# Performance work log

Hardware: AMD Instinct MI355X
Metric: run time of the kernel (lower is better)

The kernel has to match this reference:

```python
import jax, jax.numpy as jnp
import numpy as np

N_NODES = 100000
N_EDGES = 1600000
N_GRAPHS = 1000
NODES_PER_GRAPH = 100  # batch vector is arange(N)//100: exactly 100 nodes per graph
HID = 32
MAX_Z = 1000
K = 30
D_LAT = HID * 3 + 1  # 97, total_latent_dim


def setup_inputs() -> dict:
    key = jax.random.key(0)
    ks = jax.random.split(key, 24)
    s = 1.0 / np.sqrt(HID)
    inp = {
        "z": jax.random.randint(ks[0], (N_NODES,), 0, MAX_Z, dtype=jnp.int32),
        "edge_index": jax.random.randint(ks[1], (2, N_EDGES), 0, N_NODES, dtype=jnp.int32),
        "batch": (jnp.arange(N_NODES, dtype=jnp.int32) // NODES_PER_GRAPH),
        "edge_weight": jax.random.uniform(ks[2], (N_EDGES,), jnp.float32, 0.1, 1.0),
        "z_emb": jax.random.normal(ks[3], (MAX_Z, HID), jnp.float32) * 0.1,
        # GCNConv stack: [32->32, 32->32, 32->32, 32->1]
        "Wg1": jax.random.normal(ks[4], (HID, HID)) * s,
        "bg1": jnp.zeros((HID,), jnp.float32),
        "Wg2": jax.random.normal(ks[5], (HID, HID)) * s,
        "bg2": jnp.zeros((HID,), jnp.float32),
        "Wg3": jax.random.normal(ks[6], (HID, HID)) * s,
        "bg3": jnp.zeros((HID,), jnp.float32),
        "Wg4": jax.random.normal(ks[7], (HID, 1)) * s,
        "bg4": jnp.zeros((1,), jnp.float32),
        # Conv1d(1, 16, kernel=97, stride=97)
        "Wc1": jax.random.normal(ks[8], (16, D_LAT)) * (1.0 / np.sqrt(D_LAT)),
        "bc1": jnp.zeros((16,), jnp.float32),
        # Conv1d(16, 32, kernel=5, stride=1)
        "Wc2": jax.random.normal(ks[9], (32, 16, 5)) * (1.0 / np.sqrt(16 * 5)),
        "bc2": jnp.zeros((32,), jnp.float32),
        # Linear(352, 128), Linear(128, 1)
        "Wl1": jax.random.normal(ks[10], (352, 128)) * (1.0 / np.sqrt(352)),
        "bl1": jnp.zeros((128,), jnp.float32),
        "Wl2": jax.random.normal(ks[11], (128, 1)) * (1.0 / np.sqrt(128)),
        "bl2": jnp.zeros((1,), jnp.float32),
    }
    return inp


def gcn_conv(x, src, dst, ew, W, b, n):
    # PyG GCNConv: xW, add self-loops (weight 1), sym-normalize, aggregate at dst, + bias
    xw = x @ W
    deg = jax.ops.segment_sum(ew, dst, num_segments=n) + 1.0  # +1 for self loop
    dinv = jnp.where(deg > 0, jax.lax.rsqrt(deg), 0.0)
    norm = dinv[src] * ew * dinv[dst]                          # [E]
    out = jax.ops.segment_sum(norm[:, None] * xw[src], dst, num_segments=n)
    out = out + xw * (dinv * dinv)[:, None]                    # self-loop term
    return out + b


def _forward(z, edge_index, batch, edge_weight, z_emb, Wg1, bg1, Wg2, bg2, Wg3, bg3,
             Wg4, bg4, Wc1, bc1, Wc2, bc2, Wl1, bl1, Wl2, bl2):
    src, dst = edge_index[0], edge_index[1]
    n = z.shape[0]
    x = z_emb[z]                                              # [N, 32]
    xs = []
    h = x
    for W, b in ((Wg1, bg1), (Wg2, bg2), (Wg3, bg3), (Wg4, bg4)):
        h = jnp.tanh(gcn_conv(h, src, dst, edge_weight, W, b, n))
        xs.append(h)
    x = jnp.concatenate(xs, axis=-1)                          # [N, 97]
    # global_sort_pool: batch is uniform (100 nodes/graph) so dense batching is a reshape
    dense = x.reshape(N_GRAPHS, NODES_PER_GRAPH, D_LAT)       # [B, 100, 97]
    idx = jnp.argsort(-dense[:, :, -1], axis=1)[:, :K]        # sort desc by last channel
    top = jnp.take_along_axis(dense, idx[:, :, None], axis=1)  # [B, 30, 97]
    # Conv1d(1,16,97,stride=97) on flattened [B,1,30*97] == per-slot dense layer
    y = jax.nn.relu(jnp.einsum('bkd,cd->bck', top, Wc1) + bc1[None, :, None])  # [B,16,30]
    y = y.reshape(N_GRAPHS, 16, K // 2, 2).max(axis=-1)        # MaxPool1d(2,2) -> [B,16,15]
    y = jax.lax.conv_general_dilated(y, Wc2, (1,), 'VALID',
                                     dimension_numbers=('NCH', 'OIH', 'NCH'))
    y = jax.nn.relu(y + bc2[None, :, None])                    # [B,32,11]
    y = y.reshape(N_GRAPHS, -1)                                # [B,352]
    y = jax.nn.relu(y @ Wl1 + bl1)                             # dropout: eval mode, identity
    return y @ Wl2 + bl2                                       # [B,1]


def reference(z, edge_index, batch, edge_weight, z_emb, Wg1, bg1, Wg2, bg2, Wg3, bg3,
              Wg4, bg4, Wc1, bc1, Wc2, bc2, Wl1, bl1, Wl2, bl2):
    return _forward(z, edge_index, batch, edge_weight, z_emb, Wg1, bg1, Wg2, bg2, Wg3,
                    bg3, Wg4, bg4, Wc1, bc1, Wc2, bc2, Wl1, bl1, Wl2, bl2)
```

## Files before the change

### kernel.cpp

```cpp
#include <hip/hip_runtime.h>

#define HID 32
#define DLAT 97
#define NPG 100
#define TOPK 30
#define BKT_NODES 128
#define BKT_SHIFT 7
#define NBUCK 1024
#define CAPF 2432
#define CHUNK 8192

typedef float f32x4 __attribute__((ext_vector_type(4)));

__device__ __forceinline__ f32x4 gload4(const float* p) {
    f32x4 r;
    asm volatile("global_load_dwordx4 %0, %1, off" : "=v"(r) : "v"(p));
    return r;
}

__global__ __launch_bounds__(512) void binB1_kernel(
    const int* __restrict__ src, const int* __restrict__ dst,
    const float* __restrict__ ew, int* __restrict__ gcursor,
    int2* __restrict__ bedge, int E) {
    __shared__ int hist[NBUCK];
    __shared__ int lcur[NBUCK];
    __shared__ int dcache[CHUNK];
    for (int i = threadIdx.x; i < NBUCK; i += 512) hist[i] = 0;
    __syncthreads();
    int base = blockIdx.x * CHUNK;
    int M = min(E - base, CHUNK);
    for (int i = threadIdx.x; i < M; i += 512) {
        int d = dst[base + i];
        dcache[i] = d;
        atomicAdd(&hist[d >> BKT_SHIFT], 1);
    }
    __syncthreads();
    for (int b = threadIdx.x; b < NBUCK; b += 512) {
        int v = hist[b];
        lcur[b] = b * CAPF + (v ? atomicAdd(&gcursor[b], v) : 0);
    }
    __syncthreads();
    for (int i = threadIdx.x; i < M; i += 512) {
        int d = dcache[i];
        int slot = atomicAdd(&lcur[d >> BKT_SHIFT], 1);
        bedge[slot] = make_int2(src[base + i] | ((d & (BKT_NODES - 1)) << 20),
                                __float_as_int(ew[base + i]));
    }
}

__global__ __launch_bounds__(256) void scan1024_kernel(
    const int* __restrict__ g, int* __restrict__ bstart) {
    __shared__ int sh[256];
    int t = threadIdx.x;
    int t4 = t * 4;
    int a0 = g[t4], a1 = g[t4 + 1], a2 = g[t4 + 2], a3 = g[t4 + 3];
    int tsum = a0 + a1 + a2 + a3;
    sh[t] = tsum;
    __syncthreads();
    for (int off = 1; off < 256; off <<= 1) {
        int tv = (t >= off) ? sh[t - off] : 0;
        __syncthreads();
        sh[t] += tv;
        __syncthreads();
    }
    int e = sh[t] - tsum;
    bstart[t4] = e;
    bstart[t4 + 1] = e + a0;
    bstart[t4 + 2] = e + a0 + a1;
    bstart[t4 + 3] = e + a0 + a1 + a2;
}

__global__ __launch_bounds__(512) void sortlocal3_kernel(
    const int2* __restrict__ bedge, const int* __restrict__ gcursor,
    const int* __restrict__ bstart,
    const int* __restrict__ z, const float* __restrict__ z_emb,
    const float* __restrict__ W1, int2* __restrict__ csr,
    int* __restrict__ row_start, int* __restrict__ row_deg,
    float* __restrict__ dinv, float* __restrict__ xw_a, int N) {
    __shared__ int2 LDSe[CAPF];
    __shared__ int cnt[BKT_NODES];
    __shared__ int sh2[BKT_NODES];
    __shared__ int lc2[BKT_NODES];
    __shared__ int zloc[BKT_NODES];
    __shared__ float wsum[BKT_NODES];
    __shared__ float dloc[BKT_NODES];
    __shared__ float W1L[HID * HID];

    int b = blockIdx.x, t = threadIdx.x;
    for (int i = t; i < HID * HID; i += 512) W1L[i] = W1[i];
    if (t < BKT_NODES) { cnt[t] = 0; wsum[t] = 0.f; }
    __syncthreads();

    const int begOut = bstart[b];
    const int M = gcursor[b];

    for (int i = t; i < M; i += 512) {
        int2 e = bedge[(size_t)b * CAPF + i];
        LDSe[i] = e;
        int nl = (e.x >> 20) & (BKT_NODES - 1);
        atomicAdd(&cnt[nl], 1);
        atomicAdd(&wsum[nl], __int_as_float(e.y));
    }
    __syncthreads();
    int v = 0, excl = 0;
    int n = b * BKT_NODES + t;
    if (t < BKT_NODES) { v = cnt[t]; sh2[t] = v; }
    __syncthreads();
    for (int off = 1; off < BKT_NODES; off <<= 1) {
        int tv = (t >= off && t < BKT_NODES) ? sh2[t - off] : 0;
        __syncthreads();
        if (t < BKT_NODES) sh2[t] += tv;
        __syncthreads();
    }
    if (t < BKT_NODES) {
        excl = sh2[t] - v;
        lc2[t] = excl;
        float di = 1.f / sqrtf(1.f + wsum[t]);
        dloc[t] = di;
        if (n < N) {
            row_start[n] = begOut + excl;
            row_deg[n] = v;
            dinv[n] = di;
            zloc[t] = z[n];
        } else {
            zloc[t] = 0;
        }
    }
    __syncthreads();
    for (int i = t; i < M; i += 512) {
        int2 e = LDSe[i];
        int slot = atomicAdd(&lc2[(e.x >> 20) & (BKT_NODES - 1)], 1);
        csr[begOut + slot] = make_int2(e.x & 0xFFFFF, e.y);
    }
    int lim = min(BKT_NODES, N - b * BKT_NODES);
    if (lim > 0) {
        for (int idx = t; idx < lim * HID; idx += 512) {
            int nl = idx >> 5, f = idx & 31;
            const float* row = z_emb + (size_t)zloc[nl] * HID;
            float s = 0.f;
#pragma unroll
            for (int k = 0; k < HID; ++k) s += row[k] * W1L[k * HID + f];
            xw_a[(size_t)(b * BKT_NODES + nl) * HID + f] = s * dloc[nl];
        }
    }
}

template <int MODE>
__global__ __launch_bounds__(256) void agg32z_kernel(
    const int* __restrict__ row_start, const int* __restrict__ row_deg,
    const int2* __restrict__ csr, const float* __restrict__ xw,
    const float* __restrict__ b, const float* __restrict__ dinv,
    const float* __restrict__ Wn, float* __restrict__ cout,
    float* __restrict__ xw_next, int N) {
    __shared__ float WnL[HID * HID];
    int t = threadIdx.x;
    if (MODE == 0) {
        for (int i = t; i < HID * HID; i += 256) WnL[i] = Wn[i];
    } else {
        if (t < HID) WnL[t] = Wn[t];
    }
    __syncthreads();
    int tid = blockIdx.x * 256 + t;
    int n = tid >> 5;
    if (n >= N) return;
    int lane = t & 31;
    int eq = lane & 3;
    int f4 = lane & 28;
    int beg = row_start[n];
    int deg = row_deg[n];
    float di = dinv[n];
    float selfv = xw[(size_t)n * HID + lane];
    int end = beg + deg;
    float4 acc = make_float4(0.f, 0.f, 0.f, 0.f);
    for (int i = beg; i < end; i += 32) {
        int e = i + lane;
        int2 ce = csr[min(e, end - 1)];
        float we = (e < end) ? __int_as_float(ce.y) : 0.f;
        int ci = ce.x;
        int jmax = min(8, (end - i + 3) >> 2);
        f32x4 x[8];
        float w[8];
#pragma unroll
        for (int j = 0; j < 8; ++j) {
            if (j < jmax) {
                int s = 4 * j + eq;
                int idx = __shfl(ci, s, 32);
                w[j] = __shfl(we, s, 32);
                x[j] = gload4(xw + (size_t)idx * HID + f4);
            }
        }
        asm volatile("s_waitcnt vmcnt(0)" ::: "memory");
        __builtin_amdgcn_sched_barrier(0);
#pragma unroll
        for (int j = 0; j < 8; ++j) {
            if (j < jmax) {
                acc.x += w[j] * x[j].x;
                acc.y += w[j] * x[j].y;
                acc.z += w[j] * x[j].z;
                acc.w += w[j] * x[j].w;
            }
        }
    }
#pragma unroll
    for (int m = 1; m <= 2; m <<= 1) {
        acc.x += __shfl_xor(acc.x, m, 32);
        acc.y += __shfl_xor(acc.y, m, 32);
        acc.z += __shfl_xor(acc.z, m, 32);
        acc.w += __shfl_xor(acc.w, m, 32);
    }
    float s = (eq == 0) ? acc.x : (eq == 1) ? acc.y : (eq == 2) ? acc.z : acc.w;
    float outv = tanhf(di * (s + selfv) + b[lane]);
    cout[(size_t)n * HID + lane] = outv;

    if (MODE == 0) {
        float p = 0.f;
#pragma unroll
        for (int k = 0; k < HID; ++k) {
            float ok = __shfl(outv, k, 32);
            p += ok * WnL[k * HID + lane];
        }
        xw_next[(size_t)n * HID + lane] = p * di;
    } else {
        float p = outv * WnL[lane];
        p += __shfl_xor(p, 16, 32);
        p += __shfl_xor(p, 8, 32);
        p += __shfl_xor(p, 4, 32);
        p += __shfl_xor(p, 2, 32);
        p += __shfl_xor(p, 1, 32);
        if (lane == 0) xw_next[n] = p * di;
    }
}

__global__ __launch_bounds__(256) void topk_head_kernel(
    const int* __restrict__ row_start, const int* __restrict__ row_deg,
    const int2* __restrict__ csr, const float* __restrict__ xw4,
    const float* __restrict__ b4, const float* __restrict__ dinv,
    const float* __restrict__ cblk,
    const float* __restrict__ Wc1, const float* __restrict__ bc1,
    const float* __restrict__ Wc2, const float* __restrict__ bc2,
    const float* __restrict__ Wl1, const float* __restrict__ bl1,
    const float* __restrict__ Wl2, const float* __restrict__ bl2,
    float* __restrict__ out, int N) {
    int g = blockIdx.x;
    int tid = threadIdx.x;
    __shared__ float v[NPG];
    __shared__ int tidx[TOPK];
    __shared__ float tval[TOPK];
    __shared__ float top[TOPK * DLAT];
    __shared__ float Wc1L[16 * DLAT];
    __shared__ float Wc2L[32 * 16 * 5];
    __shared__ float y1[16 * TOPK];
    __shared__ float y2[16 * 15];
    __shared__ float y3[352];
    __shared__ float r[256];

    for (int i = tid; i < 16 * DLAT; i += 256) Wc1L[i] = Wc1[i];
    for (int i = tid; i < 32 * 16 * 5; i += 256) Wc2L[i] = Wc2[i];

    if (tid < NPG) {
        int n = g * NPG + tid;
        int beg = row_start[n], end = beg + row_deg[n];
        float s0 = 0.f, s1 = 0.f;
        for (int i = beg; i < end; i += 4) {
            int2 e0 = csr[min(i, end - 1)];
            int2 e1 = csr[min(i + 1, end - 1)];
            int2 e2 = csr[min(i + 2, end - 1)];
            int2 e3 = csr[min(i + 3, end - 1)];
            float x0 = xw4[e0.x], x1 = xw4[e1.x], x2 = xw4[e2.x], x3 = xw4[e3.x];
            s0 += __int_as_float(e0.y) * x0;
            if (i + 1 < end) s1 += __int_as_float(e1.y) * x1;
            if (i + 2 < end) s0 += __int_as_float(e2.y) * x2;
            if (i + 3 < end) s1 += __int_as_float(e3.y) * x3;
        }
        v[tid] = tanhf(dinv[n] * ((s0 + s1) + xw4[n]) + b4[0]);
    }
    __syncthreads();
    if (tid < NPG) {
        float vi = v[tid];
        int cnt = 0;
#pragma unroll 4
        for (int j = 0; j < NPG; ++j) {
            float vj = v[j];
            cnt += (vj > vi) || (vj == vi && j < tid);
        }
        if (cnt < TOPK) {
            tidx[cnt] = g * NPG + tid;
            tval[cnt] = vi;
        }
    }
    __syncthreads();

    for (int idx = tid; idx < TOPK * 24; idx += 256) {
        int k = idx / 24, q = idx - k * 24;
        int l = q >> 3, fq = q & 7;
        const float4 val =
            *(const float4*)(cblk + (size_t)l * N * HID + (size_t)tidx[k] * HID + fq * 4);
        float* dst = top + k * DLAT + l * HID + fq * 4;
        dst[0] = val.x; dst[1] = val.y; dst[2] = val.z; dst[3] = val.w;
    }
    if (tid < TOPK) top[tid * DLAT + 96] = tval[tid];
    __syncthreads();

    for (int idx = tid; idx < 16 * TOPK; idx += 256) {
        int c = idx / TOPK, k = idx % TOPK;
        float s = bc1[c];
        const float* w = Wc1L + c * DLAT;
        const float* t = top + k * DLAT;
#pragma unroll 4
        for (int d = 0; d < DLAT; ++d) s += t[d] * w[d];
        y1[c * TOPK + k] = fmaxf(s, 0.f);
    }
    __syncthreads();

    for (int idx = tid; idx < 16 * 15; idx += 256) {
        int c = idx / 15, j = idx % 15;
        y2[idx] = fmaxf(y1[c * TOPK + 2 * j], y1[c * TOPK + 2 * j + 1]);
    }
    __syncthreads();

    for (int idx = tid; idx < 352; idx += 256) {
        int o = idx / 11, t = idx % 11;
        float s = bc2[o];
#pragma unroll
        for (int i = 0; i < 16; ++i) {
#pragma unroll
            for (int k = 0; k < 5; ++k)
                s += Wc2L[(o * 16 + i) * 5 + k] * y2[i * 15 + t + k];
        }
        y3[idx] = fmaxf(s, 0.f);
    }
    __syncthreads();

    {
        int half = tid >> 7;
        int o = tid & 127;
        int d0 = half * 176;
        float s = (half == 0) ? bl1[o] : 0.f;
#pragma unroll 1
        for (int d = d0; d < d0 + 176; d += 8) {
            float wv[8], yv[8];
#pragma unroll
            for (int j = 0; j < 8; ++j) wv[j] = Wl1[(d + j) * 128 + o];
#pragma unroll
            for (int j = 0; j < 8; ++j) yv[j] = y3[d + j];
#pragma unroll
            for (int j = 0; j < 8; ++j) s += yv[j] * wv[j];
        }
        r[tid] = s;
    }
    __syncthreads();
    if (tid < 128) r[tid] = fmaxf(r[tid] + r[tid + 128], 0.f) * Wl2[tid];
    __syncthreads();
    if (tid < 64) r[tid] += r[tid + 64];
    __syncthreads();
    if (tid == 0) {
        float s = 0.f;
        for (int j = 0; j < 64; ++j) s += r[j];
        out[g] = s + bl2[0];
    }
}


extern "C" void kernel_launch(void* const* d_in, const int* in_sizes, int n_in,
                              void* d_out, int out_size, void* d_ws, size_t ws_size,
                              hipStream_t stream) {
    const int* z = (const int*)d_in[0];
    const int* ei = (const int*)d_in[1];
    const float* ew = (const float*)d_in[3];
    const float* z_emb = (const float*)d_in[4];
    const float* Wg[4] = {(const float*)d_in[5], (const float*)d_in[7],
                          (const float*)d_in[9], (const float*)d_in[11]};
    const float* bg[4] = {(const float*)d_in[6], (const float*)d_in[8],
                          (const float*)d_in[10], (const float*)d_in[12]};
    const float* Wc1 = (const float*)d_in[13];
    const float* bc1 = (const float*)d_in[14];
    const float* Wc2 = (const float*)d_in[15];
    const float* bc2 = (const float*)d_in[16];
    const float* Wl1 = (const float*)d_in[17];
    const float* bl1 = (const float*)d_in[18];
    const float* Wl2 = (const float*)d_in[19];
    const float* bl2 = (const float*)d_in[20];
    float* out = (float*)d_out;

    const int N = in_sizes[0];
    const int E = in_sizes[1] / 2;
    const int G = out_size;
    const int* src = ei;
    const int* dst = ei + E;

    auto cdiv = [](long long a, long long b) { return (int)((a + b - 1) / b); };
    const int NB = cdiv(E, CHUNK);
    const int NBKT = cdiv(N, BKT_NODES);

    char* ws = (char*)d_ws;
    int2* bedge = (int2*)ws;                  ws += sizeof(int2) * (size_t)NBUCK * CAPF;
    int2* csr = (int2*)ws;                    ws += sizeof(int2) * (size_t)E;
    int* gcursor = (int*)ws;                  ws += sizeof(int) * NBUCK;
    int* bstart = (int*)ws;                   ws += sizeof(int) * NBUCK;
    int* row_start = (int*)ws;                ws += sizeof(int) * N;
    int* row_deg = (int*)ws;                  ws += sizeof(int) * N;
    float* dinv = (float*)ws;                 ws += sizeof(float) * N;
    float* xw_a = (float*)ws;                 ws += sizeof(float) * (size_t)N * HID;
    float* cblk = (float*)ws;                 ws += sizeof(float) * (size_t)3 * N * HID;
    float* xw4 = (float*)ws;                  ws += sizeof(float) * N;
    float* xw_b = (float*)bedge;
    float* cb0 = cblk;
    float* cb1 = cblk + (size_t)N * HID;
    float* cb2 = cblk + (size_t)2 * N * HID;

    hipMemsetAsync(gcursor, 0, sizeof(int) * NBUCK, stream);
    binB1_kernel<<<NB, 512, 0, stream>>>(src, dst, ew, gcursor, bedge, E);
    scan1024_kernel<<<1, 256, 0, stream>>>(gcursor, bstart);
    sortlocal3_kernel<<<NBKT, 512, 0, stream>>>(bedge, gcursor, bstart, z, z_emb, Wg[0],
                                                csr, row_start, row_deg, dinv, xw_a, N);

    const int AGGB = cdiv((long long)N * 32, 256);
    agg32z_kernel<0><<<AGGB, 256, 0, stream>>>(row_start, row_deg, csr, xw_a, bg[0],
                                               dinv, Wg[1], cb0, xw_b, N);
    agg32z_kernel<0><<<AGGB, 256, 0, stream>>>(row_start, row_deg, csr, xw_b, bg[1],
                                               dinv, Wg[2], cb1, xw_a, N);
    agg32z_kernel<1><<<AGGB, 256, 0, stream>>>(row_start, row_deg, csr, xw_a, bg[2],
                                               dinv, Wg[3], cb2, xw4, N);

    topk_head_kernel<<<G, 256, 0, stream>>>(row_start, row_deg, csr, xw4, bg[3], dinv,
                                            cblk, Wc1, bc1, Wc2, bc2, Wl1, bl1,
                                            Wl2, bl2, out, N);
}
```

Baseline: 346.8 us.

## Pad top-k latent rows, vectorize conv1 dot, use wave-shuffle scan, halve CHUNK

Pads the top-k latent and Wc1 rows in shared memory from 97 to 100 floats so the Conv1d(1,16) dot product can use float4 loads and stores, with zeroed padding. Replaces the barrier-heavy shared-memory prefix scan in the local sort kernel with a 64-lane wave shuffle scan plus a two-entry cross-wave fixup. Also halves the binning chunk size, which changes shared-memory use and occupancy in the binning kernel. These touch small head and sort stages, so the effect on total time is likely limited, and the CHUNK change could go either way.

After: 361.4 us. 1.04x slower.

```diff
diff --git a/kernel.cpp b/kernel.cpp
--- a/kernel.cpp
+++ b/kernel.cpp
@@ -2,13 +2,14 @@
 
 #define HID 32
 #define DLAT 97
+#define DPAD 100
 #define NPG 100
 #define TOPK 30
 #define BKT_NODES 128
 #define BKT_SHIFT 7
 #define NBUCK 1024
 #define CAPF 2432
-#define CHUNK 8192
+#define CHUNK 4096
 
 typedef float f32x4 __attribute__((ext_vector_type(4)));
 
@@ -79,12 +80,12 @@
     float* __restrict__ dinv, float* __restrict__ xw_a, int N) {
     __shared__ int2 LDSe[CAPF];
     __shared__ int cnt[BKT_NODES];
-    __shared__ int sh2[BKT_NODES];
     __shared__ int lc2[BKT_NODES];
     __shared__ int zloc[BKT_NODES];
     __shared__ float wsum[BKT_NODES];
     __shared__ float dloc[BKT_NODES];
     __shared__ float W1L[HID * HID];
+    __shared__ int wtot[2];
 
     int b = blockIdx.x, t = threadIdx.x;
     for (int i = t; i < HID * HID; i += 512) W1L[i] = W1[i];
@@ -102,18 +103,23 @@
         atomicAdd(&wsum[nl], __int_as_float(e.y));
     }
     __syncthreads();
-    int v = 0, excl = 0;
+    int v = 0, incl = 0;
     int n = b * BKT_NODES + t;
-    if (t < BKT_NODES) { v = cnt[t]; sh2[t] = v; }
-    __syncthreads();
-    for (int off = 1; off < BKT_NODES; off <<= 1) {
-        int tv = (t >= off && t < BKT_NODES) ? sh2[t - off] : 0;
-        __syncthreads();
-        if (t < BKT_NODES) sh2[t] += tv;
-        __syncthreads();
-    }
     if (t < BKT_NODES) {
-        excl = sh2[t] - v;
+        v = cnt[t];
+        incl = v;
+        int lane = t & 63;
+#pragma unroll
+        for (int off = 1; off < 64; off <<= 1) {
+            int u = __shfl_up(incl, off, 64);
+            if (lane >= off) incl += u;
+        }
+        if (lane == 63) wtot[t >> 6] = incl;
+    }
+    __syncthreads();
+    if (t < BKT_NODES) {
+        if (t >= 64) incl += wtot[0];
+        int excl = incl - v;
         lc2[t] = excl;
         float di = 1.f / sqrtf(1.f + wsum[t]);
         dloc[t] = di;
@@ -246,16 +252,20 @@
     __shared__ float v[NPG];
     __shared__ int tidx[TOPK];
     __shared__ float tval[TOPK];
-    __shared__ float top[TOPK * DLAT];
-    __shared__ float Wc1L[16 * DLAT];
+    __shared__ float top[TOPK * DPAD];
+    __shared__ float Wc1L[16 * DPAD];
     __shared__ float Wc2L[32 * 16 * 5];
     __shared__ float y1[16 * TOPK];
     __shared__ float y2[16 * 15];
     __shared__ float y3[352];
     __shared__ float r[256];
 
-    for (int i = tid; i < 16 * DLAT; i += 256) Wc1L[i] = Wc1[i];
+    for (int i = tid; i < 16 * DPAD; i += 256) {
+        int c = i / DPAD, d = i - c * DPAD;
+        Wc1L[i] = (d < DLAT) ? Wc1[c * DLAT + d] : 0.f;
+    }
     for (int i = tid; i < 32 * 16 * 5; i += 256) Wc2L[i] = Wc2[i];
+    if (tid < TOPK * 3) top[(tid / 3) * DPAD + DLAT + (tid % 3)] = 0.f;
 
     if (tid < NPG) {
         int n = g * NPG + tid;
@@ -295,19 +305,21 @@
         int l = q >> 3, fq = q & 7;
         const float4 val =
             *(const float4*)(cblk + (size_t)l * N * HID + (size_t)tidx[k] * HID + fq * 4);
-        float* dst = top + k * DLAT + l * HID + fq * 4;
-        dst[0] = val.x; dst[1] = val.y; dst[2] = val.z; dst[3] = val.w;
-    }
-    if (tid < TOPK) top[tid * DLAT + 96] = tval[tid];
+        *(float4*)(top + k * DPAD + l * HID + fq * 4) = val;
+    }
+    if (tid < TOPK) top[tid * DPAD + 96] = tval[tid];
     __syncthreads();
 
     for (int idx = tid; idx < 16 * TOPK; idx += 256) {
         int c = idx / TOPK, k = idx % TOPK;
+        const float4* w = (const float4*)(Wc1L + c * DPAD);
+        const float4* tp = (const float4*)(top + k * DPAD);
         float s = bc1[c];
-        const float* w = Wc1L + c * DLAT;
-        const float* t = top + k * DLAT;
-#pragma unroll 4
-        for (int d = 0; d < DLAT; ++d) s += t[d] * w[d];
+#pragma unroll
+        for (int d4 = 0; d4 < 25; ++d4) {
+            float4 a = tp[d4], bw = w[d4];
+            s += a.x * bw.x + a.y * bw.y + a.z * bw.z + a.w * bw.w;
+        }
         y1[c * TOPK + k] = fmaxf(s, 0.f);
     }
     __syncthreads();
```
